# Optimization experiments

Hardware: AMD Instinct MI355X
Metric: run time of the kernel (lower is better)

## Reference

```python
import jax, jax.numpy as jnp
import numpy as np

NUM_RANGES = 256
DOPPLER = 64
EMBED = 16
MAX_ELE = 37
MAX_AZI = 107
K_PER_RANGE = 512
IN_DIM = DOPPLER + 2 * EMBED  # 96


def setup_inputs() -> dict:
    key = jax.random.key(0)
    ks = jax.random.split(key, 12)
    N = NUM_RANGES * K_PER_RANGE
    s = 1.0 / np.sqrt(IN_DIM)  # torch Linear default init scale
    return {
        "power_vals": jax.random.normal(ks[0], (N, DOPPLER), dtype=jnp.float32),
        "ele_indices": jax.random.randint(ks[1], (N,), 0, MAX_ELE, dtype=jnp.int32),
        "range_indices": jax.random.randint(ks[2], (N,), 0, NUM_RANGES, dtype=jnp.int32),
        "azi_indices": jax.random.randint(ks[3], (N,), 0, MAX_AZI, dtype=jnp.int32),
        "ele_table": jax.random.normal(ks[4], (MAX_ELE, EMBED), dtype=jnp.float32),
        "azi_table": jax.random.normal(ks[5], (MAX_AZI, EMBED), dtype=jnp.float32),
        "Wq": jax.random.uniform(ks[6], (DOPPLER, IN_DIM), jnp.float32, -s, s),
        "bq": jax.random.uniform(ks[7], (DOPPLER,), jnp.float32, -s, s),
        "Wk": jax.random.uniform(ks[8], (DOPPLER, IN_DIM), jnp.float32, -s, s),
        "bk": jax.random.uniform(ks[9], (DOPPLER,), jnp.float32, -s, s),
        "Wv": jax.random.uniform(ks[10], (DOPPLER, IN_DIM), jnp.float32, -s, s),
        "bv": jax.random.uniform(ks[11], (DOPPLER,), jnp.float32, -s, s),
    }


def reference(power_vals, ele_indices, range_indices, azi_indices,
              ele_table, azi_table, Wq, bq, Wk, bk, Wv, bv):
    Kp = power_vals.shape[0] // NUM_RANGES
    # embedding gather + concat: [R, K, D + 2E]
    ele_e = ele_table[ele_indices.reshape(NUM_RANGES, Kp)]
    azi_e = azi_table[azi_indices.reshape(NUM_RANGES, Kp)]
    pv = power_vals.reshape(NUM_RANGES, Kp, DOPPLER)
    x = jnp.concatenate([pv, ele_e, azi_e], axis=-1)
    # QKV projections (torch Linear: x @ W.T + b)
    Q = jnp.einsum('rkf,df->rkd', x, Wq) + bq
    Kt = jnp.einsum('rkf,df->rkd', x, Wk) + bk
    V = jnp.einsum('rkf,df->rkd', x, Wv) + bv
    scores = jnp.einsum('rqd,rkd->rqk', Q, Kt) / jnp.sqrt(jnp.float32(DOPPLER))
    attn = jax.nn.softmax(scores, axis=-1)
    attended = jnp.einsum('rqk,rkd->rqd', attn, V)
    attended_sum = attended.sum(axis=-1)  # [R, K]
    return attended_sum.reshape(-1)
```

## Files before the change

### kernel.cpp

```cpp
#include <hip/hip_runtime.h>


#define SCALE 0.18033688011112042f

typedef __bf16 bf16;
typedef bf16 v4bf __attribute__((ext_vector_type(4)));
typedef bf16 v8bf __attribute__((ext_vector_type(8)));
typedef float v4f __attribute__((ext_vector_type(4)));

__device__ __forceinline__ v8bf pk8(float4 a, float4 b) {
    v8bf r;
    r[0] = (bf16)a.x; r[1] = (bf16)a.y; r[2] = (bf16)a.z; r[3] = (bf16)a.w;
    r[4] = (bf16)b.x; r[5] = (bf16)b.y; r[6] = (bf16)b.z; r[7] = (bf16)b.w;
    return r;
}
__device__ __forceinline__ float d4(float4 a, v4f w) {
    return a.x * w[0] + a.y * w[1] + a.z * w[2] + a.w * w[3];
}

__global__ __launch_bounds__(1024, 4)
void sda_kernel(const float* __restrict__ power,
                const int*   __restrict__ ele_i,
                const int*   __restrict__ azi_i,
                const float* __restrict__ ele_t,
                const float* __restrict__ azi_t,
                const float* __restrict__ Wq, const float* __restrict__ bq,
                const float* __restrict__ Wk, const float* __restrict__ bk,
                const float* __restrict__ Wv, const float* __restrict__ bv,
                float* __restrict__ out)
{
    extern __shared__ char smem[];
    char*  Kb   = smem;
    float* vsum = (float*)(smem + 65536);
    float* wvs  = (float*)(smem + 67584);

    const int tid  = threadIdx.x;
    const int wave = tid >> 6;
    const int lane = tid & 63;
    const int l15  = lane & 15;
    const int quad = lane >> 4;
    const int rowbase = blockIdx.x * 512 + wave * 32;

    if (tid < 96) {
        float s = 0.f;
#pragma unroll 8
        for (int r = 0; r < 64; r++) s += Wv[r * 96 + tid];
        wvs[tid] = s;
    } else if (tid == 96) {
        float s = 0.f;
#pragma unroll
        for (int d = 0; d < 64; d++) s += bv[d];
        wvs[96] = s;
    }
    __syncthreads();

    v4f w0 = *(const v4f*)(wvs + quad * 8);
    v4f w1 = *(const v4f*)(wvs + quad * 8 + 4);
    v4f w2 = *(const v4f*)(wvs + 32 + quad * 8);
    v4f w3 = *(const v4f*)(wvs + 32 + quad * 8 + 4);
    v4f w4 = *(const v4f*)(wvs + 64 + quad * 8);
    v4f w5 = *(const v4f*)(wvs + 64 + quad * 8 + 4);
    const float bvs = wvs[96];

    v8bf xa[2][3];
#pragma unroll
    for (int mt = 0; mt < 2; mt++) {
        int row = rowbase + mt * 16 + l15;
        const float* pr = power + (size_t)row * 64;
        float4 a0 = *(const float4*)(pr + quad * 8);
        float4 a1 = *(const float4*)(pr + quad * 8 + 4);
        float4 a2 = *(const float4*)(pr + 32 + quad * 8);
        float4 a3 = *(const float4*)(pr + 32 + quad * 8 + 4);
        int ie = ele_i[row];
        int ia = azi_i[row];
        const float* tb = (quad < 2) ? (ele_t + ie * 16 + quad * 8)
                                     : (azi_t + ia * 16 + (quad - 2) * 8);
        float4 a4 = *(const float4*)tb;
        float4 a5 = *(const float4*)(tb + 4);
        xa[mt][0] = pk8(a0, a1);
        xa[mt][1] = pk8(a2, a3);
        xa[mt][2] = pk8(a4, a5);
        float d = d4(a0, w0) + d4(a1, w1) + d4(a2, w2) + d4(a3, w3) + d4(a4, w4) + d4(a5, w5);
        d += __shfl_xor(d, 16);
        d += __shfl_xor(d, 32);
        if (quad == 0) vsum[wave * 32 + mt * 16 + l15] = d + bvs;
    }

    char* Sw = Kb + wave * 4096;
#pragma unroll
    for (int mtd = 0; mtd < 4; mtd++) {
        v8bf wq3[3];
#pragma unroll
        for (int kt = 0; kt < 3; kt++) {
            const float* p = Wq + (mtd * 16 + l15) * 96 + kt * 32 + quad * 8;
            wq3[kt] = pk8(*(const float4*)p, *(const float4*)(p + 4));
        }
        float4 bq4 = *(const float4*)(bq + mtd * 16 + quad * 4);
#pragma unroll
        for (int ntr = 0; ntr < 2; ntr++) {
            v4f acc = {0.f, 0.f, 0.f, 0.f};
#pragma unroll
            for (int kt = 0; kt < 3; kt++)
                acc = __builtin_amdgcn_mfma_f32_16x16x32_bf16(wq3[kt], xa[ntr][kt], acc, 0, 0, 0);
            int row = ntr * 16 + l15;
            v4bf o;
            o[0] = (bf16)((acc[0] + bq4.x) * SCALE);
            o[1] = (bf16)((acc[1] + bq4.y) * SCALE);
            o[2] = (bf16)((acc[2] + bq4.z) * SCALE);
            o[3] = (bf16)((acc[3] + bq4.w) * SCALE);
            *(v4bf*)(Sw + row * 128 +
                     ((((mtd * 2 + (quad >> 1)) ^ (row & 7)) << 4) | ((quad & 1) << 3))) = o;
        }
    }
    v8bf qf[2][2];
#pragma unroll
    for (int nt = 0; nt < 2; nt++)
#pragma unroll
        for (int kt = 0; kt < 2; kt++)
            qf[nt][kt] = *(const v8bf*)(Sw + (nt * 16 + l15) * 128 +
                                        (((kt * 4 + quad) ^ (l15 & 7)) << 4));

#pragma unroll
    for (int mtd = 0; mtd < 4; mtd++) {
        v8bf wk3[3];
#pragma unroll
        for (int kt = 0; kt < 3; kt++) {
            const float* p = Wk + (mtd * 16 + l15) * 96 + kt * 32 + quad * 8;
            wk3[kt] = pk8(*(const float4*)p, *(const float4*)(p + 4));
        }
        float4 bk4 = *(const float4*)(bk + mtd * 16 + quad * 4);
#pragma unroll
        for (int ntr = 0; ntr < 2; ntr++) {
            v4f acc = {0.f, 0.f, 0.f, 0.f};
#pragma unroll
            for (int kt = 0; kt < 3; kt++)
                acc = __builtin_amdgcn_mfma_f32_16x16x32_bf16(wk3[kt], xa[ntr][kt], acc, 0, 0, 0);
            int keyb = wave * 32 + ntr * 16 + l15;
            v4bf o;
            o[0] = (bf16)(acc[0] + bk4.x);
            o[1] = (bf16)(acc[1] + bk4.y);
            o[2] = (bf16)(acc[2] + bk4.z);
            o[3] = (bf16)(acc[3] + bk4.w);
            *(v4bf*)(Kb + keyb * 128 +
                     ((((mtd * 2 + (quad >> 1)) ^ (keyb & 7)) << 4) | ((quad & 1) << 3))) = o;
        }
    }
    __syncthreads();

    float osum[2] = {0.f, 0.f};
    float lsum[2] = {0.f, 0.f};
#pragma unroll 2
    for (int t = 0; t < 16; t++) {
        v8bf kf[2][2];
#pragma unroll
        for (int mtk = 0; mtk < 2; mtk++)
#pragma unroll
            for (int kt = 0; kt < 2; kt++) {
                int key = t * 32 + mtk * 16 + l15;
                kf[mtk][kt] = *(const v8bf*)(Kb + key * 128 + (((kt * 4 + quad) ^ (key & 7)) << 4));
            }
        v4f vs[2];
#pragma unroll
        for (int mtk = 0; mtk < 2; mtk++)
            vs[mtk] = *(const v4f*)(vsum + t * 32 + mtk * 16 + quad * 4);
#pragma unroll
        for (int mtk = 0; mtk < 2; mtk++) {
#pragma unroll
            for (int nt = 0; nt < 2; nt++) {
                v4f acc = {0.f, 0.f, 0.f, 0.f};
                acc = __builtin_amdgcn_mfma_f32_16x16x32_bf16(kf[mtk][0], qf[nt][0], acc, 0, 0, 0);
                acc = __builtin_amdgcn_mfma_f32_16x16x32_bf16(kf[mtk][1], qf[nt][1], acc, 0, 0, 0);
                float p0 = __builtin_amdgcn_exp2f(acc[0]);
                float p1 = __builtin_amdgcn_exp2f(acc[1]);
                float p2 = __builtin_amdgcn_exp2f(acc[2]);
                float p3 = __builtin_amdgcn_exp2f(acc[3]);
                lsum[nt] += (p0 + p1) + (p2 + p3);
                osum[nt] += ((p0 * vs[mtk][0] + p1 * vs[mtk][1]) +
                             (p2 * vs[mtk][2] + p3 * vs[mtk][3]));
            }
        }
    }

#pragma unroll
    for (int nt = 0; nt < 2; nt++) {
        float lv = lsum[nt];
        lv += __shfl_xor(lv, 16);
        lv += __shfl_xor(lv, 32);
        float ov = osum[nt];
        ov += __shfl_xor(ov, 16);
        ov += __shfl_xor(ov, 32);
        if (quad == 0) out[rowbase + nt * 16 + l15] = ov / lv;
    }
}

extern "C" void kernel_launch(void* const* d_in, const int* in_sizes, int n_in,
                              void* d_out, int out_size, void* d_ws, size_t ws_size,
                              hipStream_t stream) {
    const float* power = (const float*)d_in[0];
    const int*   ele_i = (const int*)d_in[1];
    const int*   azi_i = (const int*)d_in[3];
    const float* ele_t = (const float*)d_in[4];
    const float* azi_t = (const float*)d_in[5];
    const float* Wq = (const float*)d_in[6];
    const float* bq = (const float*)d_in[7];
    const float* Wk = (const float*)d_in[8];
    const float* bk = (const float*)d_in[9];
    const float* Wv = (const float*)d_in[10];
    const float* bv = (const float*)d_in[11];
    float* out = (float*)d_out;

    const int lds_bytes = 65536 + 2048 + 512;
    (void)hipFuncSetAttribute(reinterpret_cast<const void*>(sda_kernel),
                              hipFuncAttributeMaxDynamicSharedMemorySize, lds_bytes);
    sda_kernel<<<256, 1024, lds_bytes, stream>>>(power, ele_i, azi_i, ele_t, azi_t,
                                                 Wq, bq, Wk, bk, Wv, bv, out);
}
```

Measured before the change: 129.9 us.

## Split each range's queries across two blocks with XCD-aware block swizzle

Launches 512 blocks instead of 256, with each block handling half of a range's 512 queries while still building the full K and V-sum for all keys. This spreads work across more blocks to fill the GPU's compute units better, and remaps block IDs so that partner blocks land on the same XCD, which should improve L2 reuse of the shared power rows. The cost is that K projection and the V-sum are computed twice per range. It also raises launch bounds to 8 and packs the softmax accumulators into float2 vectors.

Result: slower. 184.7 us (+42.2%).

```diff
diff --git a/kernel.cpp b/kernel.cpp
--- a/kernel.cpp
+++ b/kernel.cpp
@@ -7,6 +7,7 @@
 typedef bf16 v4bf __attribute__((ext_vector_type(4)));
 typedef bf16 v8bf __attribute__((ext_vector_type(8)));
 typedef float v4f __attribute__((ext_vector_type(4)));
+typedef float v2f __attribute__((ext_vector_type(2)));
 
 __device__ __forceinline__ v8bf pk8(float4 a, float4 b) {
     v8bf r;
@@ -18,7 +19,7 @@
     return a.x * w[0] + a.y * w[1] + a.z * w[2] + a.w * w[3];
 }
 
-__global__ __launch_bounds__(1024, 4)
+__global__ __launch_bounds__(1024, 8)
 void sda_kernel(const float* __restrict__ power,
                 const int*   __restrict__ ele_i,
                 const int*   __restrict__ azi_i,
@@ -39,7 +40,14 @@
     const int lane = tid & 63;
     const int l15  = lane & 15;
     const int quad = lane >> 4;
-    const int rowbase = blockIdx.x * 512 + wave * 32;
+
+    const int bid   = blockIdx.x;
+    const int lj    = ((bid & 7) << 6) | (bid >> 3);
+    const int range = lj >> 1;
+    const int half  = lj & 1;
+
+    const int keyrow0 = range * 512 + wave * 32;
+    const int qrow    = range * 512 + half * 256 + wave * 16 + l15;
 
     if (tid < 96) {
         float s = 0.f;
@@ -54,18 +62,10 @@
     }
     __syncthreads();
 
-    v4f w0 = *(const v4f*)(wvs + quad * 8);
-    v4f w1 = *(const v4f*)(wvs + quad * 8 + 4);
-    v4f w2 = *(const v4f*)(wvs + 32 + quad * 8);
-    v4f w3 = *(const v4f*)(wvs + 32 + quad * 8 + 4);
-    v4f w4 = *(const v4f*)(wvs + 64 + quad * 8);
-    v4f w5 = *(const v4f*)(wvs + 64 + quad * 8 + 4);
-    const float bvs = wvs[96];
-
-    v8bf xa[2][3];
+    v8bf xk[2][3];
 #pragma unroll
     for (int mt = 0; mt < 2; mt++) {
-        int row = rowbase + mt * 16 + l15;
+        int row = keyrow0 + mt * 16 + l15;
         const float* pr = power + (size_t)row * 64;
         float4 a0 = *(const float4*)(pr + quad * 8);
         float4 a1 = *(const float4*)(pr + quad * 8 + 4);
@@ -77,13 +77,36 @@
                                      : (azi_t + ia * 16 + (quad - 2) * 8);
         float4 a4 = *(const float4*)tb;
         float4 a5 = *(const float4*)(tb + 4);
-        xa[mt][0] = pk8(a0, a1);
-        xa[mt][1] = pk8(a2, a3);
-        xa[mt][2] = pk8(a4, a5);
-        float d = d4(a0, w0) + d4(a1, w1) + d4(a2, w2) + d4(a3, w3) + d4(a4, w4) + d4(a5, w5);
+        xk[mt][0] = pk8(a0, a1);
+        xk[mt][1] = pk8(a2, a3);
+        xk[mt][2] = pk8(a4, a5);
+        float d = d4(a0, *(const v4f*)(wvs + quad * 8))
+                + d4(a1, *(const v4f*)(wvs + quad * 8 + 4))
+                + d4(a2, *(const v4f*)(wvs + 32 + quad * 8))
+                + d4(a3, *(const v4f*)(wvs + 32 + quad * 8 + 4))
+                + d4(a4, *(const v4f*)(wvs + 64 + quad * 8))
+                + d4(a5, *(const v4f*)(wvs + 64 + quad * 8 + 4));
         d += __shfl_xor(d, 16);
         d += __shfl_xor(d, 32);
-        if (quad == 0) vsum[wave * 32 + mt * 16 + l15] = d + bvs;
+        if (quad == 0) vsum[wave * 32 + mt * 16 + l15] = d + wvs[96];
+    }
+
+    v8bf xq[3];
+    {
+        const float* pr = power + (size_t)qrow * 64;
+        float4 a0 = *(const float4*)(pr + quad * 8);
+        float4 a1 = *(const float4*)(pr + quad * 8 + 4);
+        float4 a2 = *(const float4*)(pr + 32 + quad * 8);
+        float4 a3 = *(const float4*)(pr + 32 + quad * 8 + 4);
+        int ie = ele_i[qrow];
+        int ia = azi_i[qrow];
+        const float* tb = (quad < 2) ? (ele_t + ie * 16 + quad * 8)
+                                     : (azi_t + ia * 16 + (quad - 2) * 8);
+        float4 a4 = *(const float4*)tb;
+        float4 a5 = *(const float4*)(tb + 4);
+        xq[0] = pk8(a0, a1);
+        xq[1] = pk8(a2, a3);
+        xq[2] = pk8(a4, a5);
     }
 
     char* Sw = Kb + wave * 4096;
@@ -96,29 +119,23 @@
             wq3[kt] = pk8(*(const float4*)p, *(const float4*)(p + 4));
         }
         float4 bq4 = *(const float4*)(bq + mtd * 16 + quad * 4);
-#pragma unroll
-        for (int ntr = 0; ntr < 2; ntr++) {
-            v4f acc = {0.f, 0.f, 0.f, 0.f};
-#pragma unroll
-            for (int kt = 0; kt < 3; kt++)
-                acc = __builtin_amdgcn_mfma_f32_16x16x32_bf16(wq3[kt], xa[ntr][kt], acc, 0, 0, 0);
-            int row = ntr * 16 + l15;
-            v4bf o;
-            o[0] = (bf16)((acc[0] + bq4.x) * SCALE);
-            o[1] = (bf16)((acc[1] + bq4.y) * SCALE);
-            o[2] = (bf16)((acc[2] + bq4.z) * SCALE);
-            o[3] = (bf16)((acc[3] + bq4.w) * SCALE);
-            *(v4bf*)(Sw + row * 128 +
-                     ((((mtd * 2 + (quad >> 1)) ^ (row & 7)) << 4) | ((quad & 1) << 3))) = o;
-        }
-    }
-    v8bf qf[2][2];
-#pragma unroll
-    for (int nt = 0; nt < 2; nt++)
-#pragma unroll
-        for (int kt = 0; kt < 2; kt++)
-            qf[nt][kt] = *(const v8bf*)(Sw + (nt * 16 + l15) * 128 +
-                                        (((kt * 4 + quad) ^ (l15 & 7)) << 4));
+        v4f acc = {0.f, 0.f, 0.f, 0.f};
+#pragma unroll
+        for (int kt = 0; kt < 3; kt++)
+            acc = __builtin_amdgcn_mfma_f32_16x16x32_bf16(wq3[kt], xq[kt], acc, 0, 0, 0);
+        int row = l15;
+        v4bf o;
+        o[0] = (bf16)((acc[0] + bq4.x) * SCALE);
+        o[1] = (bf16)((acc[1] + bq4.y) * SCALE);
+        o[2] = (bf16)((acc[2] + bq4.z) * SCALE);
+        o[3] = (bf16)((acc[3] + bq4.w) * SCALE);
+        *(v4bf*)(Sw + row * 128 +
+                 ((((mtd * 2 + (quad >> 1)) ^ (row & 7)) << 4) | ((quad & 1) << 3))) = o;
+    }
+    v8bf qf[2];
+#pragma unroll
+    for (int kt = 0; kt < 2; kt++)
+        qf[kt] = *(const v8bf*)(Sw + l15 * 128 + (((kt * 4 + quad) ^ (l15 & 7)) << 4));
 
 #pragma unroll
     for (int mtd = 0; mtd < 4; mtd++) {
@@ -134,7 +151,7 @@
             v4f acc = {0.f, 0.f, 0.f, 0.f};
 #pragma unroll
             for (int kt = 0; kt < 3; kt++)
-                acc = __builtin_amdgcn_mfma_f32_16x16x32_bf16(wk3[kt], xa[ntr][kt], acc, 0, 0, 0);
+                acc = __builtin_amdgcn_mfma_f32_16x16x32_bf16(wk3[kt], xk[ntr][kt], acc, 0, 0, 0);
             int keyb = wave * 32 + ntr * 16 + l15;
             v4bf o;
             o[0] = (bf16)(acc[0] + bk4.x);
@@ -147,8 +164,8 @@
     }
     __syncthreads();
 
-    float osum[2] = {0.f, 0.f};
-    float lsum[2] = {0.f, 0.f};
+    v2f oacc = {0.f, 0.f};
+    v2f lacc = {0.f, 0.f};
 #pragma unroll 2
     for (int t = 0; t < 16; t++) {
         v8bf kf[2][2];
@@ -165,32 +182,29 @@
             vs[mtk] = *(const v4f*)(vsum + t * 32 + mtk * 16 + quad * 4);
 #pragma unroll
         for (int mtk = 0; mtk < 2; mtk++) {
-#pragma unroll
-            for (int nt = 0; nt < 2; nt++) {
-                v4f acc = {0.f, 0.f, 0.f, 0.f};
-                acc = __builtin_amdgcn_mfma_f32_16x16x32_bf16(kf[mtk][0], qf[nt][0], acc, 0, 0, 0);
-                acc = __builtin_amdgcn_mfma_f32_16x16x32_bf16(kf[mtk][1], qf[nt][1], acc, 0, 0, 0);
-                float p0 = __builtin_amdgcn_exp2f(acc[0]);
-                float p1 = __builtin_amdgcn_exp2f(acc[1]);
-                float p2 = __builtin_amdgcn_exp2f(acc[2]);
-                float p3 = __builtin_amdgcn_exp2f(acc[3]);
-                lsum[nt] += (p0 + p1) + (p2 + p3);
-                osum[nt] += ((p0 * vs[mtk][0] + p1 * vs[mtk][1]) +
-                             (p2 * vs[mtk][2] + p3 * vs[mtk][3]));
-            }
-        }
-    }
-
-#pragma unroll
-    for (int nt = 0; nt < 2; nt++) {
-        float lv = lsum[nt];
-        lv += __shfl_xor(lv, 16);
-        lv += __shfl_xor(lv, 32);
-        float ov = osum[nt];
-        ov += __shfl_xor(ov, 16);
-        ov += __shfl_xor(ov, 32);
-        if (quad == 0) out[rowbase + nt * 16 + l15] = ov / lv;
-    }
+            v4f acc = {0.f, 0.f, 0.f, 0.f};
+            acc = __builtin_amdgcn_mfma_f32_16x16x32_bf16(kf[mtk][0], qf[0], acc, 0, 0, 0);
+            acc = __builtin_amdgcn_mfma_f32_16x16x32_bf16(kf[mtk][1], qf[1], acc, 0, 0, 0);
+            float p0 = __builtin_amdgcn_exp2f(acc[0]);
+            float p1 = __builtin_amdgcn_exp2f(acc[1]);
+            float p2 = __builtin_amdgcn_exp2f(acc[2]);
+            float p3 = __builtin_amdgcn_exp2f(acc[3]);
+            v2f p01 = {p0, p1};
+            v2f p23 = {p2, p3};
+            v2f v01 = {vs[mtk][0], vs[mtk][1]};
+            v2f v23 = {vs[mtk][2], vs[mtk][3]};
+            lacc += p01 + p23;
+            oacc += p01 * v01 + p23 * v23;
+        }
+    }
+
+    float lv = lacc[0] + lacc[1];
+    lv += __shfl_xor(lv, 16);
+    lv += __shfl_xor(lv, 32);
+    float ov = oacc[0] + oacc[1];
+    ov += __shfl_xor(ov, 16);
+    ov += __shfl_xor(ov, 32);
+    if (quad == 0) out[range * 512 + half * 256 + wave * 16 + l15] = ov / lv;
 }
 
 extern "C" void kernel_launch(void* const* d_in, const int* in_sizes, int n_in,
@@ -212,6 +226,6 @@
     const int lds_bytes = 65536 + 2048 + 512;
     (void)hipFuncSetAttribute(reinterpret_cast<const void*>(sda_kernel),
                               hipFuncAttributeMaxDynamicSharedMemorySize, lds_bytes);
-    sda_kernel<<<256, 1024, lds_bytes, stream>>>(power, ele_i, azi_i, ele_t, azi_t,
+    sda_kernel<<<512, 1024, lds_bytes, stream>>>(power, ele_i, azi_i, ele_t, azi_t,
                                                  Wq, bq, Wk, bk, Wv, bv, out);
 }
```

## Split fused attention into QKV projection and attention kernels via workspace

Applied to the files above, without the earlier changes.

Replaces the single fused kernel with two launches: one computes Q, K (bf16) and the V row-sums into global workspace, and the second loads each range's K into LDS and runs attention for half the queries per block. This doubles the grid from 256 to 512 blocks so more CUs are busy, and uses an XCD-aware block remapping. In exchange it adds a global round trip for Q/K (about 32 MB of bf16 traffic) and a second launch. The original fused kernel is kept as a fallback when the workspace is too small.

Result: slower. 161.8 us (+24.6%).

```diff
diff --git a/kernel.cpp b/kernel.cpp
--- a/kernel.cpp
+++ b/kernel.cpp
@@ -7,6 +7,7 @@
 typedef bf16 v4bf __attribute__((ext_vector_type(4)));
 typedef bf16 v8bf __attribute__((ext_vector_type(8)));
 typedef float v4f __attribute__((ext_vector_type(4)));
+typedef float v2f __attribute__((ext_vector_type(2)));
 
 __device__ __forceinline__ v8bf pk8(float4 a, float4 b) {
     v8bf r;
@@ -18,16 +19,219 @@
     return a.x * w[0] + a.y * w[1] + a.z * w[2] + a.w * w[3];
 }
 
+__global__ __launch_bounds__(1024, 8)
+void sda_qkv(const float* __restrict__ power,
+             const int*   __restrict__ ele_i,
+             const int*   __restrict__ azi_i,
+             const float* __restrict__ ele_t,
+             const float* __restrict__ azi_t,
+             const float* __restrict__ Wq, const float* __restrict__ bq,
+             const float* __restrict__ Wk, const float* __restrict__ bk,
+             const float* __restrict__ Wv, const float* __restrict__ bv,
+             bf16* __restrict__ Qg, bf16* __restrict__ Kg,
+             float* __restrict__ vsg)
+{
+    __shared__ float wvs[98];
+    __shared__ char  scratch[16 * 2048];
+
+    const int tid  = threadIdx.x;
+    const int wave = tid >> 6;
+    const int lane = tid & 63;
+    const int l15  = lane & 15;
+    const int quad = lane >> 4;
+
+    const int bid = blockIdx.x;
+    const int lj  = ((bid & 7) << 6) | (bid >> 3);
+    const int row = lj * 256 + wave * 16 + l15;
+
+    if (tid < 96) {
+        float s = 0.f;
+#pragma unroll 8
+        for (int r = 0; r < 64; r++) s += Wv[r * 96 + tid];
+        wvs[tid] = s;
+    } else if (tid == 96) {
+        float s = 0.f;
+#pragma unroll
+        for (int d = 0; d < 64; d++) s += bv[d];
+        wvs[96] = s;
+    }
+    __syncthreads();
+
+    v8bf xa[3];
+    float d;
+    {
+        const float* pr = power + (size_t)row * 64;
+        float4 a0 = *(const float4*)(pr + quad * 8);
+        float4 a1 = *(const float4*)(pr + quad * 8 + 4);
+        xa[0] = pk8(a0, a1);
+        d  = d4(a0, *(const v4f*)(wvs + quad * 8))
+           + d4(a1, *(const v4f*)(wvs + quad * 8 + 4));
+        float4 a2 = *(const float4*)(pr + 32 + quad * 8);
+        float4 a3 = *(const float4*)(pr + 32 + quad * 8 + 4);
+        xa[1] = pk8(a2, a3);
+        d += d4(a2, *(const v4f*)(wvs + 32 + quad * 8))
+           + d4(a3, *(const v4f*)(wvs + 32 + quad * 8 + 4));
+        int ie = ele_i[row];
+        int ia = azi_i[row];
+        const float* tb = (quad < 2) ? (ele_t + ie * 16 + quad * 8)
+                                     : (azi_t + ia * 16 + (quad - 2) * 8);
+        float4 a4 = *(const float4*)tb;
+        float4 a5 = *(const float4*)(tb + 4);
+        xa[2] = pk8(a4, a5);
+        d += d4(a4, *(const v4f*)(wvs + 64 + quad * 8))
+           + d4(a5, *(const v4f*)(wvs + 64 + quad * 8 + 4));
+    }
+    d += __shfl_xor(d, 16);
+    d += __shfl_xor(d, 32);
+    if (quad == 0) vsg[row] = d + wvs[96];
+
+    char* Sw = scratch + wave * 2048;
+
+#pragma unroll 1
+    for (int mtd = 0; mtd < 4; mtd++) {
+        v8bf w3[3];
+#pragma unroll
+        for (int kt = 0; kt < 3; kt++) {
+            const float* p = Wq + (mtd * 16 + l15) * 96 + kt * 32 + quad * 8;
+            w3[kt] = pk8(*(const float4*)p, *(const float4*)(p + 4));
+        }
+        float4 b4 = *(const float4*)(bq + mtd * 16 + quad * 4);
+        v4f acc = {0.f, 0.f, 0.f, 0.f};
+#pragma unroll
+        for (int kt = 0; kt < 3; kt++)
+            acc = __builtin_amdgcn_mfma_f32_16x16x32_bf16(w3[kt], xa[kt], acc, 0, 0, 0);
+        v4bf o;
+        o[0] = (bf16)((acc[0] + b4.x) * SCALE);
+        o[1] = (bf16)((acc[1] + b4.y) * SCALE);
+        o[2] = (bf16)((acc[2] + b4.z) * SCALE);
+        o[3] = (bf16)((acc[3] + b4.w) * SCALE);
+        *(v4bf*)(Sw + l15 * 128 +
+                 ((((mtd * 2 + (quad >> 1)) ^ (l15 & 7)) << 4) | ((quad & 1) << 3))) = o;
+    }
+#pragma unroll
+    for (int kt = 0; kt < 2; kt++) {
+        v8bf q = *(const v8bf*)(Sw + l15 * 128 + (((kt * 4 + quad) ^ (l15 & 7)) << 4));
+        *(v8bf*)(Qg + (size_t)row * 64 + (kt * 4 + quad) * 8) = q;
+    }
+
+#pragma unroll 1
+    for (int mtd = 0; mtd < 4; mtd++) {
+        v8bf w3[3];
+#pragma unroll
+        for (int kt = 0; kt < 3; kt++) {
+            const float* p = Wk + (mtd * 16 + l15) * 96 + kt * 32 + quad * 8;
+            w3[kt] = pk8(*(const float4*)p, *(const float4*)(p + 4));
+        }
+        float4 b4 = *(const float4*)(bk + mtd * 16 + quad * 4);
+        v4f acc = {0.f, 0.f, 0.f, 0.f};
+#pragma unroll
+        for (int kt = 0; kt < 3; kt++)
+            acc = __builtin_amdgcn_mfma_f32_16x16x32_bf16(w3[kt], xa[kt], acc, 0, 0, 0);
+        v4bf o;
+        o[0] = (bf16)(acc[0] + b4.x);
+        o[1] = (bf16)(acc[1] + b4.y);
+        o[2] = (bf16)(acc[2] + b4.z);
+        o[3] = (bf16)(acc[3] + b4.w);
+        *(v4bf*)(Sw + l15 * 128 +
+                 ((((mtd * 2 + (quad >> 1)) ^ (l15 & 7)) << 4) | ((quad & 1) << 3))) = o;
+    }
+#pragma unroll
+    for (int kt = 0; kt < 2; kt++) {
+        v8bf k = *(const v8bf*)(Sw + l15 * 128 + (((kt * 4 + quad) ^ (l15 & 7)) << 4));
+        *(v8bf*)(Kg + (size_t)row * 64 + (kt * 4 + quad) * 8) = k;
+    }
+}
+
+__global__ __launch_bounds__(1024, 8)
+void sda_attn(const bf16* __restrict__ Qg, const bf16* __restrict__ Kg,
+              const float* __restrict__ vsg, float* __restrict__ out)
+{
+    extern __shared__ char smem[];
+    char*  Kb   = smem;
+    float* vs_l = (float*)(smem + 65536);
+
+    const int tid  = threadIdx.x;
+    const int wave = tid >> 6;
+    const int lane = tid & 63;
+    const int l15  = lane & 15;
+    const int quad = lane >> 4;
+
+    const int bid   = blockIdx.x;
+    const int lj    = ((bid & 7) << 6) | (bid >> 3);
+    const int range = lj >> 1;
+    const int half  = lj & 1;
+
+    const bf16* Ksrc = Kg + (size_t)range * 512 * 64;
+#pragma unroll
+    for (int i = 0; i < 4; i++) {
+        int c = tid + i * 1024;
+        int r = c >> 3;
+        int j = c & 7;
+        v8bf kv = *(const v8bf*)(Ksrc + r * 64 + j * 8);
+        *(v8bf*)(Kb + r * 128 + ((j ^ (r & 7)) << 4)) = kv;
+    }
+    if (tid < 512) vs_l[tid] = vsg[range * 512 + tid];
+
+    const int qrow = range * 512 + half * 256 + wave * 16 + l15;
+    v8bf qf[2];
+#pragma unroll
+    for (int kt = 0; kt < 2; kt++)
+        qf[kt] = *(const v8bf*)(Qg + (size_t)qrow * 64 + (kt * 4 + quad) * 8);
+    __syncthreads();
+
+    v2f oacc = {0.f, 0.f};
+    v2f lacc = {0.f, 0.f};
+#pragma unroll 2
+    for (int t = 0; t < 16; t++) {
+        v8bf kf[2][2];
+#pragma unroll
+        for (int mtk = 0; mtk < 2; mtk++)
+#pragma unroll
+            for (int kt = 0; kt < 2; kt++) {
+                int key = t * 32 + mtk * 16 + l15;
+                kf[mtk][kt] = *(const v8bf*)(Kb + key * 128 + (((kt * 4 + quad) ^ (key & 7)) << 4));
+            }
+        v4f vs[2];
+#pragma unroll
+        for (int mtk = 0; mtk < 2; mtk++)
+            vs[mtk] = *(const v4f*)(vs_l + t * 32 + mtk * 16 + quad * 4);
+#pragma unroll
+        for (int mtk = 0; mtk < 2; mtk++) {
+            v4f acc = {0.f, 0.f, 0.f, 0.f};
+            acc = __builtin_amdgcn_mfma_f32_16x16x32_bf16(kf[mtk][0], qf[0], acc, 0, 0, 0);
+            acc = __builtin_amdgcn_mfma_f32_16x16x32_bf16(kf[mtk][1], qf[1], acc, 0, 0, 0);
+            float p0 = __builtin_amdgcn_exp2f(acc[0]);
+            float p1 = __builtin_amdgcn_exp2f(acc[1]);
+            float p2 = __builtin_amdgcn_exp2f(acc[2]);
+            float p3 = __builtin_amdgcn_exp2f(acc[3]);
+            v2f p01 = {p0, p1};
+            v2f p23 = {p2, p3};
+            v2f v01 = {vs[mtk][0], vs[mtk][1]};
+            v2f v23 = {vs[mtk][2], vs[mtk][3]};
+            lacc += p01 + p23;
+            oacc += p01 * v01 + p23 * v23;
+        }
+    }
+
+    float lv = lacc[0] + lacc[1];
+    lv += __shfl_xor(lv, 16);
+    lv += __shfl_xor(lv, 32);
+    float ov = oacc[0] + oacc[1];
+    ov += __shfl_xor(ov, 16);
+    ov += __shfl_xor(ov, 32);
+    if (quad == 0) out[qrow] = ov / lv;
+}
+
 __global__ __launch_bounds__(1024, 4)
-void sda_kernel(const float* __restrict__ power,
-                const int*   __restrict__ ele_i,
-                const int*   __restrict__ azi_i,
-                const float* __restrict__ ele_t,
-                const float* __restrict__ azi_t,
-                const float* __restrict__ Wq, const float* __restrict__ bq,
-                const float* __restrict__ Wk, const float* __restrict__ bk,
-                const float* __restrict__ Wv, const float* __restrict__ bv,
-                float* __restrict__ out)
+void sda_mono(const float* __restrict__ power,
+              const int*   __restrict__ ele_i,
+              const int*   __restrict__ azi_i,
+              const float* __restrict__ ele_t,
+              const float* __restrict__ azi_t,
+              const float* __restrict__ Wq, const float* __restrict__ bq,
+              const float* __restrict__ Wk, const float* __restrict__ bk,
+              const float* __restrict__ Wv, const float* __restrict__ bv,
+              float* __restrict__ out)
 {
     extern __shared__ char smem[];
     char*  Kb   = smem;
@@ -209,9 +413,27 @@
     const float* bv = (const float*)d_in[11];
     float* out = (float*)d_out;
 
-    const int lds_bytes = 65536 + 2048 + 512;
-    (void)hipFuncSetAttribute(reinterpret_cast<const void*>(sda_kernel),
-                              hipFuncAttributeMaxDynamicSharedMemorySize, lds_bytes);
-    sda_kernel<<<256, 1024, lds_bytes, stream>>>(power, ele_i, azi_i, ele_t, azi_t,
-                                                 Wq, bq, Wk, bk, Wv, bv, out);
-}
+    const size_t NROWS = 131072;
+    const size_t q_bytes = NROWS * 64 * sizeof(bf16);
+    const size_t need = 2 * q_bytes + NROWS * sizeof(float);
+
+    if (ws_size >= need) {
+        bf16* Qg  = (bf16*)d_ws;
+        bf16* Kg  = Qg + NROWS * 64;
+        float* vsg = (float*)((char*)d_ws + 2 * q_bytes);
+
+        sda_qkv<<<512, 1024, 0, stream>>>(power, ele_i, azi_i, ele_t, azi_t,
+                                          Wq, bq, Wk, bk, Wv, bv, Qg, Kg, vsg);
+
+        const int lds2 = 65536 + 2048;
+        (void)hipFuncSetAttribute(reinterpret_cast<const void*>(sda_attn),
+                                  hipFuncAttributeMaxDynamicSharedMemorySize, lds2);
+        sda_attn<<<512, 1024, lds2, stream>>>(Qg, Kg, vsg, out);
+    } else {
+        const int lds_bytes = 65536 + 2048 + 512;
+        (void)hipFuncSetAttribute(reinterpret_cast<const void*>(sda_mono),
+                                  hipFuncAttributeMaxDynamicSharedMemorySize, lds_bytes);
+        sda_mono<<<256, 1024, lds_bytes, stream>>>(power, ele_i, azi_i, ele_t, azi_t,
+                                                   Wq, bq, Wk, bk, Wv, bv, out);
+    }
+}
```

## Stage bf16 Wq/Wk weights in LDS and prefetch power rows early

Applied to the files above, without the earlier changes.

The block now cooperatively converts Wq and Wk to bf16 and stores them in shared memory once, instead of every wave loading the fp32 weights from global memory and converting them. Power rows and index loads are issued before the Wv column-sum prologue so their latency overlaps it, and the projection loops are no longer unrolled to reduce register pressure. LDS use grows to about 91 KB per block, which could limit co-residency, and the extra staging adds work before the first barrier.

New measurement: 110.7 us. 14.8% less time.

```diff
diff --git a/kernel.cpp b/kernel.cpp
--- a/kernel.cpp
+++ b/kernel.cpp
@@ -33,6 +33,10 @@
     char*  Kb   = smem;
     float* vsum = (float*)(smem + 65536);
     float* wvs  = (float*)(smem + 67584);
+    bf16*  WqL  = (bf16*)(smem + 68096);
+    bf16*  WkL  = (bf16*)(smem + 80384);
+    float* bqL  = (float*)(smem + 92672);
+    float* bkL  = (float*)(smem + 92928);
 
     const int tid  = threadIdx.x;
     const int wave = tid >> 6;
@@ -41,9 +45,30 @@
     const int quad = lane >> 4;
     const int rowbase = blockIdx.x * 512 + wave * 32;
 
+    float4 A[2][4];
+    int IE[2], IA[2];
+#pragma unroll
+    for (int mt = 0; mt < 2; mt++) {
+        int row = rowbase + mt * 16 + l15;
+        const float* pr = power + (size_t)row * 64;
+        A[mt][0] = *(const float4*)(pr + quad * 8);
+        A[mt][1] = *(const float4*)(pr + quad * 8 + 4);
+        A[mt][2] = *(const float4*)(pr + 32 + quad * 8);
+        A[mt][3] = *(const float4*)(pr + 32 + quad * 8 + 4);
+        IE[mt] = ele_i[row];
+        IA[mt] = azi_i[row];
+    }
+
+#pragma unroll
+    for (int i = 0; i < 6; i++) {
+        int idx = tid + i * 1024;
+        WqL[idx] = (bf16)Wq[idx];
+        WkL[idx] = (bf16)Wk[idx];
+    }
+    if (tid < 64) { bqL[tid] = bq[tid]; bkL[tid] = bk[tid]; }
     if (tid < 96) {
         float s = 0.f;
-#pragma unroll 8
+#pragma unroll 16
         for (int r = 0; r < 64; r++) s += Wv[r * 96 + tid];
         wvs[tid] = s;
     } else if (tid == 96) {
@@ -65,37 +90,29 @@
     v8bf xa[2][3];
 #pragma unroll
     for (int mt = 0; mt < 2; mt++) {
-        int row = rowbase + mt * 16 + l15;
-        const float* pr = power + (size_t)row * 64;
-        float4 a0 = *(const float4*)(pr + quad * 8);
-        float4 a1 = *(const float4*)(pr + quad * 8 + 4);
-        float4 a2 = *(const float4*)(pr + 32 + quad * 8);
-        float4 a3 = *(const float4*)(pr + 32 + quad * 8 + 4);
-        int ie = ele_i[row];
-        int ia = azi_i[row];
-        const float* tb = (quad < 2) ? (ele_t + ie * 16 + quad * 8)
-                                     : (azi_t + ia * 16 + (quad - 2) * 8);
+        const float* tb = (quad < 2) ? (ele_t + IE[mt] * 16 + quad * 8)
+                                     : (azi_t + IA[mt] * 16 + (quad - 2) * 8);
         float4 a4 = *(const float4*)tb;
         float4 a5 = *(const float4*)(tb + 4);
-        xa[mt][0] = pk8(a0, a1);
-        xa[mt][1] = pk8(a2, a3);
+        xa[mt][0] = pk8(A[mt][0], A[mt][1]);
+        xa[mt][1] = pk8(A[mt][2], A[mt][3]);
         xa[mt][2] = pk8(a4, a5);
-        float d = d4(a0, w0) + d4(a1, w1) + d4(a2, w2) + d4(a3, w3) + d4(a4, w4) + d4(a5, w5);
+        float d = d4(A[mt][0], w0) + d4(A[mt][1], w1) + d4(A[mt][2], w2)
+                + d4(A[mt][3], w3) + d4(a4, w4) + d4(a5, w5);
         d += __shfl_xor(d, 16);
         d += __shfl_xor(d, 32);
         if (quad == 0) vsum[wave * 32 + mt * 16 + l15] = d + bvs;
     }
 
     char* Sw = Kb + wave * 4096;
-#pragma unroll
+#pragma unroll 1
     for (int mtd = 0; mtd < 4; mtd++) {
+        const bf16* wrow = WqL + (mtd * 16 + l15) * 96;
         v8bf wq3[3];
 #pragma unroll
-        for (int kt = 0; kt < 3; kt++) {
-            const float* p = Wq + (mtd * 16 + l15) * 96 + kt * 32 + quad * 8;
-            wq3[kt] = pk8(*(const float4*)p, *(const float4*)(p + 4));
-        }
-        float4 bq4 = *(const float4*)(bq + mtd * 16 + quad * 4);
+        for (int kt = 0; kt < 3; kt++)
+            wq3[kt] = *(const v8bf*)(wrow + kt * 32 + quad * 8);
+        float4 bq4 = *(const float4*)(bqL + mtd * 16 + quad * 4);
 #pragma unroll
         for (int ntr = 0; ntr < 2; ntr++) {
             v4f acc = {0.f, 0.f, 0.f, 0.f};
@@ -120,15 +137,14 @@
             qf[nt][kt] = *(const v8bf*)(Sw + (nt * 16 + l15) * 128 +
                                         (((kt * 4 + quad) ^ (l15 & 7)) << 4));
 
-#pragma unroll
+#pragma unroll 1
     for (int mtd = 0; mtd < 4; mtd++) {
+        const bf16* wrow = WkL + (mtd * 16 + l15) * 96;
         v8bf wk3[3];
 #pragma unroll
-        for (int kt = 0; kt < 3; kt++) {
-            const float* p = Wk + (mtd * 16 + l15) * 96 + kt * 32 + quad * 8;
-            wk3[kt] = pk8(*(const float4*)p, *(const float4*)(p + 4));
-        }
-        float4 bk4 = *(const float4*)(bk + mtd * 16 + quad * 4);
+        for (int kt = 0; kt < 3; kt++)
+            wk3[kt] = *(const v8bf*)(wrow + kt * 32 + quad * 8);
+        float4 bk4 = *(const float4*)(bkL + mtd * 16 + quad * 4);
 #pragma unroll
         for (int ntr = 0; ntr < 2; ntr++) {
             v4f acc = {0.f, 0.f, 0.f, 0.f};
@@ -209,7 +225,7 @@
     const float* bv = (const float*)d_in[11];
     float* out = (float*)d_out;
 
-    const int lds_bytes = 65536 + 2048 + 512;
+    const int lds_bytes = 93184;
     (void)hipFuncSetAttribute(reinterpret_cast<const void*>(sda_kernel),
                               hipFuncAttributeMaxDynamicSharedMemorySize, lds_bytes);
     sda_kernel<<<256, 1024, lds_bytes, stream>>>(power, ele_i, azi_i, ele_t, azi_t,
```
